# Optimization experiments

Hardware: AMD Instinct MI355X
Metric: run time of the kernel (lower is better)

Reference implementation:

```python
import math
import jax, jax.numpy as jnp
import numpy as np

D_MODEL = 1024
N_HEADS = 16
D_K = D_MODEL // N_HEADS
B = 8
L = 1024
LATTICE = (4, 4)
TWO_PI = 2.0 * math.pi


def _build_neighbors():
    """Replicates LatticeMultiHeadAttention._build_neighbors (Moore 8-neighborhood)."""
    positions = [divmod(i, LATTICE[1]) for i in range(N_HEADS)]
    idx = np.full((N_HEADS, 8), -1, dtype=np.int64)
    w = np.zeros((N_HEADS, 8), dtype=np.float32)
    for i, (r1, c1) in enumerate(positions):
        k = 0
        for dr in (-1, 0, 1):
            for dc in (-1, 0, 1):
                if dr == 0 and dc == 0:
                    continue
                if k >= 8:
                    break
                r2, c2 = r1 + dr, c1 + dc
                for j, (r, c) in enumerate(positions):
                    if (r, c) == (r2, c2):
                        idx[i, k] = j
                        w[i, k] = math.exp(-math.hypot(dr, dc))
                        k += 1
                        break
    return idx, w


def setup_inputs() -> dict:
    key = jax.random.key(0)
    ks = jax.random.split(key, 8)
    s = 1.0 / math.sqrt(D_MODEL)
    nbr_idx_np, nbr_w_np = _build_neighbors()
    return {
        "query": jax.random.normal(ks[0], (B, L, D_MODEL), jnp.float32),
        "key_": jax.random.normal(ks[1], (B, L, D_MODEL), jnp.float32),
        "value": jax.random.normal(ks[2], (B, L, D_MODEL), jnp.float32),
        # head-stacked projection weights, stored as [H, d_model, d_k] (x @ W)
        "Wq": jax.random.normal(ks[3], (N_HEADS, D_MODEL, D_K), jnp.float32) * s,
        "Wk": jax.random.normal(ks[4], (N_HEADS, D_MODEL, D_K), jnp.float32) * s,
        "Wv": jax.random.normal(ks[5], (N_HEADS, D_MODEL, D_K), jnp.float32) * s,
        "Wo": jax.random.normal(ks[6], (D_MODEL, D_MODEL), jnp.float32) * s,
        "bo": jax.random.normal(ks[7], (D_MODEL,), jnp.float32) * 0.01,
        # buffers: initial phases (0.0), intrinsic freqs 1 + 0.1*h, lattice tables
        "phases0": jnp.zeros((N_HEADS,), jnp.float32),
        "freqs": jnp.asarray(1.0 + 0.1 * np.arange(N_HEADS), jnp.float32),
        "nbr_w": jnp.asarray(nbr_w_np),
        "nbr_idx": jnp.asarray(nbr_idx_np),
    }


def _updated_phases(phases0, freqs, nbr_w, nbr_idx):
    # multi-head batched Kuramoto step (note: coupling_strength is NOT used here,
    # matching the original forward), then the per-head internal step (empty
    # neighbor_phases branch adds another 0.01 * intrinsic_freq).
    valid = (nbr_idx >= 0).astype(phases0.dtype)        # [H,8]
    nbr_ph = phases0[jnp.clip(nbr_idx, 0, None)] * valid  # [H,8]
    phase_diff = nbr_ph - phases0[:, None]
    force = (nbr_w * jnp.sin(phase_diff)).sum(axis=1)     # [H]
    p1 = jnp.mod(phases0 + 0.01 * (freqs + force), TWO_PI)
    p2 = jnp.mod(p1 + 0.01 * freqs, TWO_PI)
    return p2


def reference(query, key_, value, Wq, Wk, Wv, Wo, bo, phases0, freqs, nbr_w, nbr_idx):
    # phases are torch buffers updated under no_grad -> constants w.r.t. autodiff
    p2 = jax.lax.stop_gradient(
        _updated_phases(phases0, freqs, nbr_w, nbr_idx))
    bias = 0.1 * jnp.cos(p2)                               # [H]

    Q = jnp.einsum('bld,hdk->bhlk', query, Wq)
    K = jnp.einsum('bld,hdk->bhlk', key_, Wk)
    V = jnp.einsum('bld,hdk->bhlk', value, Wv)

    scores = jnp.einsum('bhlk,bhmk->bhlm', Q, K) / jnp.sqrt(
        jnp.asarray(D_K, Q.dtype))
    scores = scores + bias[None, :, None, None]
    attn = jax.nn.softmax(scores, axis=-1)                 # [B,H,L,L]
    ctx = jnp.einsum('bhlm,bhmk->bhlk', attn, V)           # [B,H,L,d_k]
    ctx = ctx.transpose(0, 2, 1, 3).reshape(query.shape[0], query.shape[1], D_MODEL)
    return ctx @ Wo + bo                                   # out_proj
```

## Files before the change

kernel.cpp:

```cpp
#include <hip/hip_runtime.h>
#include <hip/hip_bf16.h>
#include <stdint.h>


typedef unsigned short u16;
typedef __bf16 bf16_t;
typedef bf16_t bf16x8 __attribute__((ext_vector_type(8)));
typedef u16 u16x8 __attribute__((ext_vector_type(8)));
typedef float f32x4 __attribute__((ext_vector_type(4)));

#define DEVI static __device__ __forceinline__
#define MFMA16(a, b, c) __builtin_amdgcn_mfma_f32_16x16x32_bf16((a), (b), (c), 0, 0, 0)

DEVI void gload_lds16(const void* g, void* l) {
  __builtin_amdgcn_global_load_lds((__attribute__((address_space(1))) void*)g,
                                   (__attribute__((address_space(3))) void*)l, 16, 0, 0);
}

DEVI u16 f2bf(float x) {
  bf16_t b = (bf16_t)x;
  u16 u;
  __builtin_memcpy(&u, &b, 2);
  return u;
}

__global__ __launch_bounds__(256) void prep(const float* __restrict__ Wq,
                                            const float* __restrict__ Wk,
                                            const float* __restrict__ Wv,
                                            const float* __restrict__ Wo,
                                            const float* __restrict__ q,
                                            const float* __restrict__ k,
                                            const float* __restrict__ v,
                                            u16* __restrict__ ws) {
  int bx = blockIdx.x;
  if (bx < 1024) {
    __shared__ float T[64][65];
    int mat = bx >> 8, ti = bx & 255;
    int rb = ti >> 4, cb = ti & 15;
    const float* src = (mat == 0) ? Wq : (mat == 1) ? Wk : (mat == 2) ? Wv : Wo;
    u16* dst = ws + (size_t)mat * 1048576;
    int stride = (mat < 3) ? 64 : 1024;
    size_t srcBase = (mat < 3) ? ((size_t)rb * 65536 + cb * 4096)
                               : ((size_t)rb * 65536 + cb * 64);
    size_t dstBase = (mat < 3) ? ((size_t)rb * 65536 + cb * 64)
                               : ((size_t)cb * 65536 + rb * 64);
#pragma unroll
    for (int p = 0; p < 4; ++p) {
      int e = p * 256 + threadIdx.x;
      int rr = e >> 4, c4 = (e & 15) * 4;
      float4 vv = *(const float4*)(src + srcBase + (size_t)rr * stride + c4);
      T[rr][c4] = vv.x; T[rr][c4 + 1] = vv.y; T[rr][c4 + 2] = vv.z; T[rr][c4 + 3] = vv.w;
    }
    __syncthreads();
#pragma unroll
    for (int p = 0; p < 2; ++p) {
      int e = p * 256 + threadIdx.x;
      int n = e >> 3, c8 = (e & 7) * 8;
      u16x8 o;
#pragma unroll
      for (int i = 0; i < 8; ++i) o[i] = f2bf(T[c8 + i][n]);
      *(u16x8*)(dst + dstBase + (size_t)n * 1024 + c8) = o;
    }
  } else {
    int id = (bx - 1024) * 256 + threadIdx.x;
    int t = id >> 21;
    size_t rem = (size_t)(id & 2097151) * 4;
    const float* src = (t == 0) ? q : (t == 1) ? k : v;
    float4 a = *(const float4*)(src + rem);
    ushort4 st;
    st.x = f2bf(a.x); st.y = f2bf(a.y); st.z = f2bf(a.z); st.w = f2bf(a.w);
    *(ushort4*)(ws + 4194304 + (size_t)t * 8388608 + rem) = st;
  }
}

__global__ __launch_bounds__(256, 2) void gemm_qkv(const u16* __restrict__ WT,
                                                   const u16* __restrict__ X,
                                                   u16* __restrict__ Qw,
                                                   u16* __restrict__ Kw,
                                                   u16* __restrict__ Vw) {
  __shared__ __align__(1024) u16 lds[2][2][8192];
  char* ldsc = (char*)lds;
  int tid = threadIdx.x;
  int wid = tid >> 6, lane = tid & 63, quad = lane >> 4, l16 = lane & 15;
  int wm = wid >> 1, wn = wid & 1;

  int id = blockIdx.x;
  int wgid = (id & 7) * 192 + (id >> 3);
  int mt = wgid & 7;
  int rest = wgid >> 3;
  int nt = rest & 63;
  int z = rest >> 6;
  const u16* Ag = WT + (size_t)z * 1048576 + (size_t)mt * 131072;
  const u16* Bg = X + (size_t)z * 8388608 + (size_t)nt * 131072;
  u16* out = (z == 0) ? Qw : (z == 1) ? Kw : Vw;
  float oscale = (z == 0) ? 0.125f : 1.0f;

  int r0 = tid >> 3;
  int lc = (tid ^ r0) & 7;
  size_t gbase = (size_t)r0 * 1024 + lc * 8;

  int rx = l16 & 7;
  int rowA = wm * 64 + l16;
  int rowB = wn * 64 + l16;

  auto stage = [&](int buf, int kt) {
#pragma unroll
    for (int p = 0; p < 4; ++p)
      gload_lds16(Ag + gbase + (size_t)p * 32768 + kt * 64,
                  ldsc + buf * 32768 + p * 4096 + tid * 16);
#pragma unroll
    for (int p = 0; p < 4; ++p)
      gload_lds16(Bg + gbase + (size_t)p * 32768 + kt * 64,
                  ldsc + buf * 32768 + 16384 + p * 4096 + tid * 16);
  };
  auto rdA = [&](int buf, int mf, int ks) -> bf16x8 {
    return *(const bf16x8*)(ldsc + buf * 32768 + (rowA + mf * 16) * 128 +
                            ((((ks << 2) | quad) ^ rx) << 4));
  };
  auto rdB = [&](int buf, int nf, int ks) -> bf16x8 {
    return *(const bf16x8*)(ldsc + buf * 32768 + 16384 + (rowB + nf * 16) * 128 +
                            ((((ks << 2) | quad) ^ rx) << 4));
  };

  f32x4 acc[4][4];
#pragma unroll
  for (int i = 0; i < 4; ++i)
#pragma unroll
    for (int j = 0; j < 4; ++j) acc[i][j] = {0.f, 0.f, 0.f, 0.f};
  bf16x8 af[4][2], bfr[4][2];

  stage(0, 0);
  stage(1, 1);
  asm volatile("s_waitcnt vmcnt(8)" ::: "memory");
  __builtin_amdgcn_s_barrier();

  for (int t = 0; t < 16; ++t) {
    int cur = t & 1;
#pragma unroll
    for (int mf = 0; mf < 4; ++mf)
#pragma unroll
      for (int ks = 0; ks < 2; ++ks) af[mf][ks] = rdA(cur, mf, ks);
#pragma unroll
    for (int nf = 0; nf < 4; ++nf)
#pragma unroll
      for (int ks = 0; ks < 2; ++ks) bfr[nf][ks] = rdB(cur, nf, ks);
    asm volatile("s_waitcnt lgkmcnt(0)" ::: "memory");
    __builtin_amdgcn_s_barrier();
    if (t < 14) stage(cur, t + 2);
    __builtin_amdgcn_s_setprio(1);
#pragma unroll
    for (int ks = 0; ks < 2; ++ks)
#pragma unroll
      for (int mf = 0; mf < 4; ++mf)
#pragma unroll
        for (int nf = 0; nf < 4; ++nf)
          acc[mf][nf] = MFMA16(af[mf][ks], bfr[nf][ks], acc[mf][nf]);
    __builtin_amdgcn_s_setprio(0);
    if (t < 14)
      asm volatile("s_waitcnt vmcnt(8)" ::: "memory");
    else
      asm volatile("s_waitcnt vmcnt(0)" ::: "memory");
    __builtin_amdgcn_s_barrier();
  }

#pragma unroll
  for (int mf = 0; mf < 4; ++mf) {
    int m = mt * 128 + wm * 64 + mf * 16 + quad * 4;
    int h = m >> 6, dk = m & 63;
#pragma unroll
    for (int nf = 0; nf < 4; ++nf) {
      int n = nt * 128 + wn * 64 + nf * 16 + l16;
      int bb = n >> 10, l = n & 1023;
      f32x4 vv = acc[mf][nf];
      if (z < 2) {
        ushort4 st;
        st.x = f2bf(vv[0] * oscale); st.y = f2bf(vv[1] * oscale);
        st.z = f2bf(vv[2] * oscale); st.w = f2bf(vv[3] * oscale);
        *(ushort4*)(out + ((size_t)((bb * 16 + h) * 1024 + l) * 64 + dk)) = st;
      } else {
        size_t base = ((size_t)((bb * 16 + h) * 64 + dk)) * 1024 + l;
        out[base] = f2bf(vv[0]);
        out[base + 1024] = f2bf(vv[1]);
        out[base + 2048] = f2bf(vv[2]);
        out[base + 3072] = f2bf(vv[3]);
      }
    }
  }
}

__global__ __launch_bounds__(256, 2) void gemm_out(const u16* __restrict__ A,
                                                   const u16* __restrict__ Bx,
                                                   float* __restrict__ outf,
                                                   const float* __restrict__ bias) {
  __shared__ __align__(1024) u16 lds[2][2][8192];
  char* ldsc = (char*)lds;
  int tid = threadIdx.x;
  int wid = tid >> 6, lane = tid & 63, quad = lane >> 4, l16 = lane & 15;
  int wm = wid >> 1, wn = wid & 1;

  int id = blockIdx.x;
  int wgid = (id & 7) * 64 + (id >> 3);
  int mt = wgid & 7;
  int nt = wgid >> 3;
  const u16* Ag = A + (size_t)mt * 131072;
  const u16* Bg = Bx + (size_t)nt * 131072;

  int r0 = tid >> 3;
  int lc = (tid ^ r0) & 7;
  size_t gbase = (size_t)r0 * 1024 + lc * 8;
  int rx = l16 & 7;
  int rowA = wm * 64 + l16;
  int rowB = wn * 64 + l16;

  auto stage = [&](int buf, int kt) {
#pragma unroll
    for (int p = 0; p < 4; ++p)
      gload_lds16(Ag + gbase + (size_t)p * 32768 + kt * 64,
                  ldsc + buf * 32768 + p * 4096 + tid * 16);
#pragma unroll
    for (int p = 0; p < 4; ++p)
      gload_lds16(Bg + gbase + (size_t)p * 32768 + kt * 64,
                  ldsc + buf * 32768 + 16384 + p * 4096 + tid * 16);
  };
  auto rdA = [&](int buf, int mf, int ks) -> bf16x8 {
    return *(const bf16x8*)(ldsc + buf * 32768 + (rowA + mf * 16) * 128 +
                            ((((ks << 2) | quad) ^ rx) << 4));
  };
  auto rdB = [&](int buf, int nf, int ks) -> bf16x8 {
    return *(const bf16x8*)(ldsc + buf * 32768 + 16384 + (rowB + nf * 16) * 128 +
                            ((((ks << 2) | quad) ^ rx) << 4));
  };

  f32x4 acc[4][4];
#pragma unroll
  for (int i = 0; i < 4; ++i)
#pragma unroll
    for (int j = 0; j < 4; ++j) acc[i][j] = {0.f, 0.f, 0.f, 0.f};
  bf16x8 af[4][2], bfr[4][2];

  stage(0, 0);
  stage(1, 1);
  asm volatile("s_waitcnt vmcnt(8)" ::: "memory");
  __builtin_amdgcn_s_barrier();

  for (int t = 0; t < 16; ++t) {
    int cur = t & 1;
#pragma unroll
    for (int mf = 0; mf < 4; ++mf)
#pragma unroll
      for (int ks = 0; ks < 2; ++ks) af[mf][ks] = rdA(cur, mf, ks);
#pragma unroll
    for (int nf = 0; nf < 4; ++nf)
#pragma unroll
      for (int ks = 0; ks < 2; ++ks) bfr[nf][ks] = rdB(cur, nf, ks);
    asm volatile("s_waitcnt lgkmcnt(0)" ::: "memory");
    __builtin_amdgcn_s_barrier();
    if (t < 14) stage(cur, t + 2);
    __builtin_amdgcn_s_setprio(1);
#pragma unroll
    for (int ks = 0; ks < 2; ++ks)
#pragma unroll
      for (int mf = 0; mf < 4; ++mf)
#pragma unroll
        for (int nf = 0; nf < 4; ++nf)
          acc[mf][nf] = MFMA16(af[mf][ks], bfr[nf][ks], acc[mf][nf]);
    __builtin_amdgcn_s_setprio(0);
    if (t < 14)
      asm volatile("s_waitcnt vmcnt(8)" ::: "memory");
    else
      asm volatile("s_waitcnt vmcnt(0)" ::: "memory");
    __builtin_amdgcn_s_barrier();
  }

#pragma unroll
  for (int mf = 0; mf < 4; ++mf) {
    int m = mt * 128 + wm * 64 + mf * 16 + quad * 4;
    float4 bq = *(const float4*)(bias + m);
#pragma unroll
    for (int nf = 0; nf < 4; ++nf) {
      int n = nt * 128 + wn * 64 + nf * 16 + l16;
      f32x4 vv = acc[mf][nf];
      float4 st;
      st.x = vv[0] + bq.x;
      st.y = vv[1] + bq.y;
      st.z = vv[2] + bq.z;
      st.w = vv[3] + bq.w;
      *(float4*)(outf + ((size_t)n * 1024 + m)) = st;
    }
  }
}

__global__ __launch_bounds__(256, 4) void attn_k(const u16* __restrict__ Q,
                                                 const u16* __restrict__ K,
                                                 const u16* __restrict__ VT,
                                                 u16* __restrict__ CTX) {
  __shared__ __align__(16) u16 sQ[128 * 64];
  __shared__ __align__(16) u16 sK[64 * 64];
  __shared__ __align__(16) u16 sV[64 * 64];
  int tid = threadIdx.x;
  int wid = tid >> 6, lane = tid & 63, quad = lane >> 4, l16 = lane & 15;
  int id = blockIdx.x + 8 * blockIdx.y;
  int xcd = id & 7, j = id >> 3;
  int qt = j & 7;
  int bh = xcd * 16 + (j >> 3);
  const u16* Qb = Q + (size_t)bh * 65536;
  const u16* Kb = K + (size_t)bh * 65536;
  const u16* Vb = VT + (size_t)bh * 65536;
  int q0 = qt * 128;

#pragma unroll
  for (int p = 0; p < 4; p++) {
    int cl = p * 256 + tid;
    int r = cl >> 3, c = cl & 7, g = c ^ (r & 7);
    gload_lds16(Qb + (size_t)(q0 + r) * 64 + g * 8, (char*)sQ + (p * 256 + wid * 64) * 16);
  }
  __syncthreads();

  bf16x8 bq[2][2];
#pragma unroll
  for (int qf = 0; qf < 2; qf++) {
    int row = wid * 32 + qf * 16 + l16;
#pragma unroll
    for (int ks = 0; ks < 2; ks++) {
      int ch = (ks * 4 + quad) ^ (row & 7);
      bq[qf][ks] = *(const bf16x8*)((const char*)sQ + row * 128 + ch * 16);
    }
  }

  u16* sPw = sQ + wid * 2048;

  f32x4 oacc[4][2];
#pragma unroll
  for (int i = 0; i < 4; i++) {
    oacc[i][0] = {0.f, 0.f, 0.f, 0.f};
    oacc[i][1] = {0.f, 0.f, 0.f, 0.f};
  }
  float lsum[2] = {0.f, 0.f};

  for (int lk0 = 0; lk0 < 1024; lk0 += 64) {
#pragma unroll
    for (int p = 0; p < 2; p++) {
      int cl = p * 256 + tid;
      int r = cl >> 3, c = cl & 7, g = c ^ (r & 7);
      gload_lds16(Kb + (size_t)(lk0 + r) * 64 + g * 8, (char*)sK + (p * 256 + wid * 64) * 16);
      gload_lds16(Vb + (size_t)r * 1024 + lk0 + g * 8, (char*)sV + (p * 256 + wid * 64) * 16);
    }
    __syncthreads();

    f32x4 s[4][2];
#pragma unroll
    for (int mt = 0; mt < 4; mt++) {
      s[mt][0] = {0.f, 0.f, 0.f, 0.f};
      s[mt][1] = {0.f, 0.f, 0.f, 0.f};
    }
#pragma unroll
    for (int ks = 0; ks < 2; ks++) {
#pragma unroll
      for (int mt = 0; mt < 4; mt++) {
        int row = mt * 16 + l16;
        int ch = (ks * 4 + quad) ^ (row & 7);
        bf16x8 a = *(const bf16x8*)((const char*)sK + row * 128 + ch * 16);
        s[mt][0] = MFMA16(a, bq[0][ks], s[mt][0]);
        s[mt][1] = MFMA16(a, bq[1][ks], s[mt][1]);
      }
    }

#pragma unroll
    for (int qf = 0; qf < 2; qf++) {
      int row = qf * 16 + l16;
#pragma unroll
      for (int mt = 0; mt < 4; mt++) {
        float p0 = __expf(s[mt][qf][0]);
        float p1 = __expf(s[mt][qf][1]);
        float p2 = __expf(s[mt][qf][2]);
        float p3 = __expf(s[mt][qf][3]);
        lsum[qf] += (p0 + p1) + (p2 + p3);
        ushort4 st;
        st.x = f2bf(p0); st.y = f2bf(p1); st.z = f2bf(p2); st.w = f2bf(p3);
        int ch = (2 * mt + (quad >> 1)) ^ (row & 7);
        *(ushort4*)((char*)sPw + row * 128 + ch * 16 + (quad & 1) * 8) = st;
      }
    }
    asm volatile("s_waitcnt lgkmcnt(0)" ::: "memory");

    bf16x8 bp[2][2];
#pragma unroll
    for (int qf = 0; qf < 2; qf++) {
      int row = qf * 16 + l16;
#pragma unroll
      for (int c = 0; c < 2; c++) {
        int ch = (c * 4 + quad) ^ (row & 7);
        bp[qf][c] = *(const bf16x8*)((const char*)sPw + row * 128 + ch * 16);
      }
    }
#pragma unroll
    for (int c = 0; c < 2; c++) {
#pragma unroll
      for (int mt = 0; mt < 4; mt++) {
        int row = mt * 16 + l16;
        int ch = (c * 4 + quad) ^ (row & 7);
        bf16x8 a = *(const bf16x8*)((const char*)sV + row * 128 + ch * 16);
        oacc[mt][0] = MFMA16(a, bp[0][c], oacc[mt][0]);
        oacc[mt][1] = MFMA16(a, bp[1][c], oacc[mt][1]);
      }
    }
    __syncthreads();
  }

#pragma unroll
  for (int qf = 0; qf < 2; qf++) {
    lsum[qf] += __shfl_xor(lsum[qf], 16, 64);
    lsum[qf] += __shfl_xor(lsum[qf], 32, 64);
  }
  float inv0 = 1.f / lsum[0], inv1 = 1.f / lsum[1];

  int b = bh >> 4, h = bh & 15;
#pragma unroll
  for (int qf = 0; qf < 2; qf++) {
    int qg = q0 + wid * 32 + qf * 16 + l16;
    float inv = qf ? inv1 : inv0;
#pragma unroll
    for (int mt = 0; mt < 4; mt++) {
      int dk = mt * 16 + quad * 4;
      ushort4 st;
      st.x = f2bf(oacc[mt][qf][0] * inv);
      st.y = f2bf(oacc[mt][qf][1] * inv);
      st.z = f2bf(oacc[mt][qf][2] * inv);
      st.w = f2bf(oacc[mt][qf][3] * inv);
      *(ushort4*)(CTX + (((size_t)(b * 1024 + qg) * 16 + h) * 64 + dk)) = st;
    }
  }
}

extern "C" void kernel_launch(void* const* d_in, const int* in_sizes, int n_in,
                              void* d_out, int out_size, void* d_ws, size_t ws_size,
                              hipStream_t stream) {
  (void)in_sizes; (void)n_in; (void)out_size;
  const float* query = (const float*)d_in[0];
  const float* key_ = (const float*)d_in[1];
  const float* value = (const float*)d_in[2];
  const float* Wq = (const float*)d_in[3];
  const float* Wk = (const float*)d_in[4];
  const float* Wv = (const float*)d_in[5];
  const float* Wo = (const float*)d_in[6];
  const float* bo = (const float*)d_in[7];

  u16* ws = (u16*)d_ws;
  u16* WT = ws;
  u16* X = ws + 4194304;
  u16* Qw = ws + 29360128;
  u16* Kw = ws + 37748736;
  u16* Vw = ws + 46137344;
  u16* Cw = X;
  float* outp = (float*)d_out;

  prep<<<25600, 256, 0, stream>>>(Wq, Wk, Wv, Wo, query, key_, value, ws);
  gemm_qkv<<<dim3(1536), 256, 0, stream>>>(WT, X, Qw, Kw, Vw);
  attn_k<<<dim3(8, 128), 256, 0, stream>>>(Qw, Kw, Vw, Cw);
  gemm_out<<<dim3(512), 256, 0, stream>>>(WT + 3145728, Cw, outp, bo);
}
```

Measured before the change: 277.6 us.

## Fuse fp32-to-bf16 activation conversion into QKV GEMM B-tile loading

Drops the separate prep pass that converted query/key/value to bf16 in workspace. The QKV GEMM now loads fp32 activations straight into registers, converts them, and writes swizzled bf16 tiles to LDS, with prefetch three k-tiles ahead. The main loop is split into two MFMA halves so the LDS writes overlap compute. This removes a full write and re-read of about 50 MB of bf16 activations. In exchange it doubles the B-operand global read bytes per GEMM tile and raises register pressure.

```diff
diff --git a/kernel.cpp b/kernel.cpp
--- a/kernel.cpp
+++ b/kernel.cpp
@@ -28,53 +28,41 @@
                                             const float* __restrict__ Wk,
                                             const float* __restrict__ Wv,
                                             const float* __restrict__ Wo,
-                                            const float* __restrict__ q,
-                                            const float* __restrict__ k,
-                                            const float* __restrict__ v,
                                             u16* __restrict__ ws) {
+  __shared__ float T[64][65];
   int bx = blockIdx.x;
-  if (bx < 1024) {
-    __shared__ float T[64][65];
-    int mat = bx >> 8, ti = bx & 255;
-    int rb = ti >> 4, cb = ti & 15;
-    const float* src = (mat == 0) ? Wq : (mat == 1) ? Wk : (mat == 2) ? Wv : Wo;
-    u16* dst = ws + (size_t)mat * 1048576;
-    int stride = (mat < 3) ? 64 : 1024;
-    size_t srcBase = (mat < 3) ? ((size_t)rb * 65536 + cb * 4096)
-                               : ((size_t)rb * 65536 + cb * 64);
-    size_t dstBase = (mat < 3) ? ((size_t)rb * 65536 + cb * 64)
-                               : ((size_t)cb * 65536 + rb * 64);
-#pragma unroll
-    for (int p = 0; p < 4; ++p) {
-      int e = p * 256 + threadIdx.x;
-      int rr = e >> 4, c4 = (e & 15) * 4;
-      float4 vv = *(const float4*)(src + srcBase + (size_t)rr * stride + c4);
-      T[rr][c4] = vv.x; T[rr][c4 + 1] = vv.y; T[rr][c4 + 2] = vv.z; T[rr][c4 + 3] = vv.w;
-    }
-    __syncthreads();
-#pragma unroll
-    for (int p = 0; p < 2; ++p) {
-      int e = p * 256 + threadIdx.x;
-      int n = e >> 3, c8 = (e & 7) * 8;
-      u16x8 o;
-#pragma unroll
-      for (int i = 0; i < 8; ++i) o[i] = f2bf(T[c8 + i][n]);
-      *(u16x8*)(dst + dstBase + (size_t)n * 1024 + c8) = o;
-    }
-  } else {
-    int id = (bx - 1024) * 256 + threadIdx.x;
-    int t = id >> 21;
-    size_t rem = (size_t)(id & 2097151) * 4;
-    const float* src = (t == 0) ? q : (t == 1) ? k : v;
-    float4 a = *(const float4*)(src + rem);
-    ushort4 st;
-    st.x = f2bf(a.x); st.y = f2bf(a.y); st.z = f2bf(a.z); st.w = f2bf(a.w);
-    *(ushort4*)(ws + 4194304 + (size_t)t * 8388608 + rem) = st;
+  int mat = bx >> 8, ti = bx & 255;
+  int rb = ti >> 4, cb = ti & 15;
+  const float* src = (mat == 0) ? Wq : (mat == 1) ? Wk : (mat == 2) ? Wv : Wo;
+  u16* dst = ws + (size_t)mat * 1048576;
+  int stride = (mat < 3) ? 64 : 1024;
+  size_t srcBase = (mat < 3) ? ((size_t)rb * 65536 + cb * 4096)
+                             : ((size_t)rb * 65536 + cb * 64);
+  size_t dstBase = (mat < 3) ? ((size_t)rb * 65536 + cb * 64)
+                             : ((size_t)cb * 65536 + rb * 64);
+#pragma unroll
+  for (int p = 0; p < 4; ++p) {
+    int e = p * 256 + threadIdx.x;
+    int rr = e >> 4, c4 = (e & 15) * 4;
+    float4 vv = *(const float4*)(src + srcBase + (size_t)rr * stride + c4);
+    T[rr][c4] = vv.x; T[rr][c4 + 1] = vv.y; T[rr][c4 + 2] = vv.z; T[rr][c4 + 3] = vv.w;
+  }
+  __syncthreads();
+#pragma unroll
+  for (int p = 0; p < 2; ++p) {
+    int e = p * 256 + threadIdx.x;
+    int n = e >> 3, c8 = (e & 7) * 8;
+    u16x8 o;
+#pragma unroll
+    for (int i = 0; i < 8; ++i) o[i] = f2bf(T[c8 + i][n]);
+    *(u16x8*)(dst + dstBase + (size_t)n * 1024 + c8) = o;
   }
 }
 
 __global__ __launch_bounds__(256, 2) void gemm_qkv(const u16* __restrict__ WT,
-                                                   const u16* __restrict__ X,
+                                                   const float* __restrict__ qf,
+                                                   const float* __restrict__ kf,
+                                                   const float* __restrict__ vf,
                                                    u16* __restrict__ Qw,
                                                    u16* __restrict__ Kw,
                                                    u16* __restrict__ Vw) {
@@ -91,27 +79,25 @@
   int nt = rest & 63;
   int z = rest >> 6;
   const u16* Ag = WT + (size_t)z * 1048576 + (size_t)mt * 131072;
-  const u16* Bg = X + (size_t)z * 8388608 + (size_t)nt * 131072;
+  const float* Bg = ((z == 0) ? qf : (z == 1) ? kf : vf) + (size_t)nt * 131072;
   u16* out = (z == 0) ? Qw : (z == 1) ? Kw : Vw;
   float oscale = (z == 0) ? 0.125f : 1.0f;
 
   int r0 = tid >> 3;
-  int lc = (tid ^ r0) & 7;
-  size_t gbase = (size_t)r0 * 1024 + lc * 8;
+  int lcA = (tid ^ r0) & 7;
+  size_t gbaseA = (size_t)r0 * 1024 + lcA * 8;
+  int c8f = (tid & 7) * 8;
+  int wxor = (((tid & 7) ^ (r0 & 7)) << 4);
 
   int rx = l16 & 7;
   int rowA = wm * 64 + l16;
   int rowB = wn * 64 + l16;
 
-  auto stage = [&](int buf, int kt) {
+  auto stageA = [&](int buf, int kt) {
 #pragma unroll
     for (int p = 0; p < 4; ++p)
-      gload_lds16(Ag + gbase + (size_t)p * 32768 + kt * 64,
+      gload_lds16(Ag + gbaseA + (size_t)p * 32768 + kt * 64,
                   ldsc + buf * 32768 + p * 4096 + tid * 16);
-#pragma unroll
-    for (int p = 0; p < 4; ++p)
-      gload_lds16(Bg + gbase + (size_t)p * 32768 + kt * 64,
-                  ldsc + buf * 32768 + 16384 + p * 4096 + tid * 16);
   };
   auto rdA = [&](int buf, int mf, int ks) -> bf16x8 {
     return *(const bf16x8*)(ldsc + buf * 32768 + (rowA + mf * 16) * 128 +
@@ -128,40 +114,96 @@
 #pragma unroll
     for (int j = 0; j < 4; ++j) acc[i][j] = {0.f, 0.f, 0.f, 0.f};
   bf16x8 af[4][2], bfr[4][2];
-
-  stage(0, 0);
-  stage(1, 1);
-  asm volatile("s_waitcnt vmcnt(8)" ::: "memory");
+  float4 fa[8], fb[8];
+
+#define ISSUE_F(KT, F)                                                        \
+  do {                                                                        \
+    _Pragma("unroll") for (int s = 0; s < 4; ++s) {                           \
+      const float* gp = Bg + (size_t)(s * 32 + r0) * 1024 + (KT) * 64 + c8f;  \
+      F[2 * s] = *(const float4*)gp;                                          \
+      F[2 * s + 1] = *(const float4*)(gp + 4);                                \
+    }                                                                         \
+  } while (0)
+
+#define WRITE_B(BUF, F)                                                       \
+  do {                                                                        \
+    _Pragma("unroll") for (int s = 0; s < 4; ++s) {                           \
+      u16x8 o;                                                                \
+      o[0] = f2bf(F[2 * s].x); o[1] = f2bf(F[2 * s].y);                       \
+      o[2] = f2bf(F[2 * s].z); o[3] = f2bf(F[2 * s].w);                       \
+      o[4] = f2bf(F[2 * s + 1].x); o[5] = f2bf(F[2 * s + 1].y);               \
+      o[6] = f2bf(F[2 * s + 1].z); o[7] = f2bf(F[2 * s + 1].w);               \
+      *(u16x8*)(ldsc + (BUF) * 32768 + 16384 + (s * 32 + r0) * 128 + wxor) = o; \
+    }                                                                         \
+  } while (0)
+
+  ISSUE_F(0, fa);
+  ISSUE_F(1, fb);
+  stageA(0, 0);
+  stageA(1, 1);
+  asm volatile("s_waitcnt vmcnt(16)" ::: "memory");
+  WRITE_B(0, fa);
+  ISSUE_F(2, fa);
+  asm volatile("s_waitcnt vmcnt(16)" ::: "memory");
+  WRITE_B(1, fb);
+  asm volatile("s_waitcnt vmcnt(12)" ::: "memory");
+  asm volatile("s_waitcnt lgkmcnt(0)" ::: "memory");
   __builtin_amdgcn_s_barrier();
 
-  for (int t = 0; t < 16; ++t) {
-    int cur = t & 1;
-#pragma unroll
-    for (int mf = 0; mf < 4; ++mf)
-#pragma unroll
-      for (int ks = 0; ks < 2; ++ks) af[mf][ks] = rdA(cur, mf, ks);
-#pragma unroll
-    for (int nf = 0; nf < 4; ++nf)
-#pragma unroll
-      for (int ks = 0; ks < 2; ++ks) bfr[nf][ks] = rdB(cur, nf, ks);
-    asm volatile("s_waitcnt lgkmcnt(0)" ::: "memory");
-    __builtin_amdgcn_s_barrier();
-    if (t < 14) stage(cur, t + 2);
-    __builtin_amdgcn_s_setprio(1);
-#pragma unroll
-    for (int ks = 0; ks < 2; ++ks)
-#pragma unroll
-      for (int mf = 0; mf < 4; ++mf)
-#pragma unroll
-        for (int nf = 0; nf < 4; ++nf)
-          acc[mf][nf] = MFMA16(af[mf][ks], bfr[nf][ks], acc[mf][nf]);
-    __builtin_amdgcn_s_setprio(0);
-    if (t < 14)
-      asm volatile("s_waitcnt vmcnt(8)" ::: "memory");
-    else
-      asm volatile("s_waitcnt vmcnt(0)" ::: "memory");
-    __builtin_amdgcn_s_barrier();
-  }
+#define QKV_ITER(T, FC, FI)                                                   \
+  do {                                                                        \
+    constexpr int t_ = (T);                                                   \
+    constexpr int cur = t_ & 1;                                               \
+    if (t_ < 13) ISSUE_F(t_ + 3, FI);                                         \
+    _Pragma("unroll") for (int mf = 0; mf < 4; ++mf)                          \
+        af[mf][0] = rdA(cur, mf, 0);                                          \
+    _Pragma("unroll") for (int nf = 0; nf < 4; ++nf)                          \
+        bfr[nf][0] = rdB(cur, nf, 0);                                         \
+    _Pragma("unroll") for (int mf = 0; mf < 4; ++mf)                          \
+        af[mf][1] = rdA(cur, mf, 1);                                          \
+    _Pragma("unroll") for (int nf = 0; nf < 4; ++nf)                          \
+        bfr[nf][1] = rdB(cur, nf, 1);                                         \
+    _Pragma("unroll") for (int mf = 0; mf < 4; ++mf)                          \
+        _Pragma("unroll") for (int nf = 0; nf < 4; ++nf)                      \
+            acc[mf][nf] = MFMA16(af[mf][0], bfr[nf][0], acc[mf][nf]);         \
+    asm volatile("s_waitcnt lgkmcnt(0)" ::: "memory");                        \
+    __builtin_amdgcn_s_barrier();                                             \
+    if (t_ < 14) stageA(cur, t_ + 2);                                         \
+    if (t_ < 13)                                                              \
+      asm volatile("s_waitcnt vmcnt(12)" ::: "memory");                       \
+    else if (t_ == 13)                                                        \
+      asm volatile("s_waitcnt vmcnt(4)" ::: "memory");                        \
+    else                                                                      \
+      asm volatile("s_waitcnt vmcnt(0)" ::: "memory");                        \
+    if (t_ < 14) WRITE_B(cur, FC);                                            \
+    __builtin_amdgcn_s_setprio(1);                                            \
+    _Pragma("unroll") for (int mf = 0; mf < 4; ++mf)                          \
+        _Pragma("unroll") for (int nf = 0; nf < 4; ++nf)                      \
+            acc[mf][nf] = MFMA16(af[mf][1], bfr[nf][1], acc[mf][nf]);         \
+    __builtin_amdgcn_s_setprio(0);                                            \
+    asm volatile("s_waitcnt lgkmcnt(0)" ::: "memory");                        \
+    __builtin_amdgcn_s_barrier();                                             \
+  } while (0)
+
+  QKV_ITER(0, fa, fb);
+  QKV_ITER(1, fb, fa);
+  QKV_ITER(2, fa, fb);
+  QKV_ITER(3, fb, fa);
+  QKV_ITER(4, fa, fb);
+  QKV_ITER(5, fb, fa);
+  QKV_ITER(6, fa, fb);
+  QKV_ITER(7, fb, fa);
+  QKV_ITER(8, fa, fb);
+  QKV_ITER(9, fb, fa);
+  QKV_ITER(10, fa, fb);
+  QKV_ITER(11, fb, fa);
+  QKV_ITER(12, fa, fb);
+  QKV_ITER(13, fb, fa);
+  QKV_ITER(14, fa, fb);
+  QKV_ITER(15, fb, fa);
+#undef QKV_ITER
+#undef ISSUE_F
+#undef WRITE_B
 
 #pragma unroll
   for (int mf = 0; mf < 4; ++mf) {
@@ -447,15 +489,14 @@
 
   u16* ws = (u16*)d_ws;
   u16* WT = ws;
-  u16* X = ws + 4194304;
+  u16* Cw = ws + 4194304;
   u16* Qw = ws + 29360128;
   u16* Kw = ws + 37748736;
   u16* Vw = ws + 46137344;
-  u16* Cw = X;
   float* outp = (float*)d_out;
 
-  prep<<<25600, 256, 0, stream>>>(Wq, Wk, Wv, Wo, query, key_, value, ws);
-  gemm_qkv<<<dim3(1536), 256, 0, stream>>>(WT, X, Qw, Kw, Vw);
+  prep<<<1024, 256, 0, stream>>>(Wq, Wk, Wv, Wo, ws);
+  gemm_qkv<<<dim3(1536), 256, 0, stream>>>(WT, query, key_, value, Qw, Kw, Vw);
   attn_k<<<dim3(8, 128), 256, 0, stream>>>(Qw, Kw, Vw, Cw);
   gemm_out<<<dim3(512), 256, 0, stream>>>(WT + 3145728, Cw, outp, bo);
 }
```

Result: slower. 307.5 us (+10.7%).

## Double-buffer K tiles and overlap V loads with QK compute in attention

Applied to the files above, without the earlier changes.

The attention kernel now keeps two K tiles in LDS and prefetches K two tiles ahead. The V tile load is issued at the start of each iteration so it overlaps the QK^T MFMAs and the softmax exponentials. The full __syncthreads are replaced by explicit vmcnt/lgkmcnt waits plus s_barrier, and s_setprio raises wave priority around the MFMA blocks. This aims to hide global-to-LDS latency behind compute, at the cost of 8 KB more LDS per block, which could lower occupancy.

```diff
diff --git a/kernel.cpp b/kernel.cpp
--- a/kernel.cpp
+++ b/kernel.cpp
@@ -295,7 +295,7 @@
                                                  const u16* __restrict__ VT,
                                                  u16* __restrict__ CTX) {
   __shared__ __align__(16) u16 sQ[128 * 64];
-  __shared__ __align__(16) u16 sK[64 * 64];
+  __shared__ __align__(16) u16 sK[2][64 * 64];
   __shared__ __align__(16) u16 sV[64 * 64];
   int tid = threadIdx.x;
   int wid = tid >> 6, lane = tid & 63, quad = lane >> 4, l16 = lane & 15;
@@ -308,13 +308,35 @@
   const u16* Vb = VT + (size_t)bh * 65536;
   int q0 = qt * 128;
 
+  auto stageK = [&](int buf, int lk0) {
+#pragma unroll
+    for (int p = 0; p < 2; ++p) {
+      int cl = p * 256 + tid;
+      int r = cl >> 3, c = cl & 7, g = c ^ (r & 7);
+      gload_lds16(Kb + (size_t)(lk0 + r) * 64 + g * 8,
+                  (char*)sK + buf * 8192 + (p * 256 + wid * 64) * 16);
+    }
+  };
+  auto stageV = [&](int lk0) {
+#pragma unroll
+    for (int p = 0; p < 2; ++p) {
+      int cl = p * 256 + tid;
+      int r = cl >> 3, c = cl & 7, g = c ^ (r & 7);
+      gload_lds16(Vb + (size_t)r * 1024 + lk0 + g * 8,
+                  (char*)sV + (p * 256 + wid * 64) * 16);
+    }
+  };
+
 #pragma unroll
   for (int p = 0; p < 4; p++) {
     int cl = p * 256 + tid;
     int r = cl >> 3, c = cl & 7, g = c ^ (r & 7);
     gload_lds16(Qb + (size_t)(q0 + r) * 64 + g * 8, (char*)sQ + (p * 256 + wid * 64) * 16);
   }
-  __syncthreads();
+  stageK(0, 0);
+  stageK(1, 64);
+  asm volatile("s_waitcnt vmcnt(2)" ::: "memory");
+  __builtin_amdgcn_s_barrier();
 
   bf16x8 bq[2][2];
 #pragma unroll
@@ -337,15 +359,9 @@
   }
   float lsum[2] = {0.f, 0.f};
 
-  for (int lk0 = 0; lk0 < 1024; lk0 += 64) {
-#pragma unroll
-    for (int p = 0; p < 2; p++) {
-      int cl = p * 256 + tid;
-      int r = cl >> 3, c = cl & 7, g = c ^ (r & 7);
-      gload_lds16(Kb + (size_t)(lk0 + r) * 64 + g * 8, (char*)sK + (p * 256 + wid * 64) * 16);
-      gload_lds16(Vb + (size_t)r * 1024 + lk0 + g * 8, (char*)sV + (p * 256 + wid * 64) * 16);
-    }
-    __syncthreads();
+  for (int t = 0; t < 16; ++t) {
+    int cur = t & 1;
+    stageV(t * 64);
 
     f32x4 s[4][2];
 #pragma unroll
@@ -353,17 +369,19 @@
       s[mt][0] = {0.f, 0.f, 0.f, 0.f};
       s[mt][1] = {0.f, 0.f, 0.f, 0.f};
     }
+    __builtin_amdgcn_s_setprio(1);
 #pragma unroll
     for (int ks = 0; ks < 2; ks++) {
 #pragma unroll
       for (int mt = 0; mt < 4; mt++) {
         int row = mt * 16 + l16;
         int ch = (ks * 4 + quad) ^ (row & 7);
-        bf16x8 a = *(const bf16x8*)((const char*)sK + row * 128 + ch * 16);
+        bf16x8 a = *(const bf16x8*)((const char*)sK + cur * 8192 + row * 128 + ch * 16);
         s[mt][0] = MFMA16(a, bq[0][ks], s[mt][0]);
         s[mt][1] = MFMA16(a, bq[1][ks], s[mt][1]);
       }
     }
+    __builtin_amdgcn_s_setprio(0);
 
 #pragma unroll
     for (int qf = 0; qf < 2; qf++) {
@@ -382,7 +400,6 @@
       }
     }
     asm volatile("s_waitcnt lgkmcnt(0)" ::: "memory");
-
     bf16x8 bp[2][2];
 #pragma unroll
     for (int qf = 0; qf < 2; qf++) {
@@ -393,6 +410,11 @@
         bp[qf][c] = *(const bf16x8*)((const char*)sPw + row * 128 + ch * 16);
       }
     }
+    asm volatile("s_waitcnt vmcnt(0)" ::: "memory");
+    __builtin_amdgcn_s_barrier();
+    if (t < 14) stageK(cur, (t + 2) * 64);
+
+    __builtin_amdgcn_s_setprio(1);
 #pragma unroll
     for (int c = 0; c < 2; c++) {
 #pragma unroll
@@ -404,7 +426,9 @@
         oacc[mt][1] = MFMA16(a, bp[1][c], oacc[mt][1]);
       }
     }
-    __syncthreads();
+    __builtin_amdgcn_s_setprio(0);
+    asm volatile("s_waitcnt lgkmcnt(0)" ::: "memory");
+    __builtin_amdgcn_s_barrier();
   }
 
 #pragma unroll
```

New measurement: 277.1 us, median of 2. About the same (-0.2%).

## Load K/V/Q fragments directly from global memory, dropping shared staging and barriers

Applied to the files above, without the earlier changes.

The attention kernel stops staging Q, K and V tiles through LDS with block-wide barriers. Each wave now reads its MFMA operands straight from global memory (relying on L1/L2 reuse across the four waves) and keeps only a small per-wave LDS buffer for the P tile. V loads are issued early to overlap with the QK^T MFMAs, and s_setprio raises wave priority around the MFMA bursts. This removes the __syncthreads and LDS traffic and shrinks LDS for higher occupancy, at the cost of redundant global/L2 reads by every wave and exposed global-load latency.

```diff
diff --git a/kernel.cpp b/kernel.cpp
--- a/kernel.cpp
+++ b/kernel.cpp
@@ -294,9 +294,7 @@
                                                  const u16* __restrict__ K,
                                                  const u16* __restrict__ VT,
                                                  u16* __restrict__ CTX) {
-  __shared__ __align__(16) u16 sQ[128 * 64];
-  __shared__ __align__(16) u16 sK[64 * 64];
-  __shared__ __align__(16) u16 sV[64 * 64];
+  __shared__ __align__(16) u16 sP[4][2048];
   int tid = threadIdx.x;
   int wid = tid >> 6, lane = tid & 63, quad = lane >> 4, l16 = lane & 15;
   int id = blockIdx.x + 8 * blockIdx.y;
@@ -306,28 +304,19 @@
   const u16* Qb = Q + (size_t)bh * 65536;
   const u16* Kb = K + (size_t)bh * 65536;
   const u16* Vb = VT + (size_t)bh * 65536;
-  int q0 = qt * 128;
-
-#pragma unroll
-  for (int p = 0; p < 4; p++) {
-    int cl = p * 256 + tid;
-    int r = cl >> 3, c = cl & 7, g = c ^ (r & 7);
-    gload_lds16(Qb + (size_t)(q0 + r) * 64 + g * 8, (char*)sQ + (p * 256 + wid * 64) * 16);
-  }
-  __syncthreads();
+  int qw = qt * 128 + wid * 32;
 
   bf16x8 bq[2][2];
 #pragma unroll
-  for (int qf = 0; qf < 2; qf++) {
-    int row = wid * 32 + qf * 16 + l16;
-#pragma unroll
-    for (int ks = 0; ks < 2; ks++) {
-      int ch = (ks * 4 + quad) ^ (row & 7);
-      bq[qf][ks] = *(const bf16x8*)((const char*)sQ + row * 128 + ch * 16);
-    }
-  }
-
-  u16* sPw = sQ + wid * 2048;
+  for (int qf = 0; qf < 2; qf++)
+#pragma unroll
+    for (int ks = 0; ks < 2; ks++)
+      bq[qf][ks] = *(const bf16x8*)(Qb + (size_t)(qw + qf * 16 + l16) * 64 +
+                                    ks * 32 + quad * 8);
+
+  u16* sPw = sP[wid];
+  const u16* Kl = Kb + (size_t)l16 * 64 + quad * 8;
+  const u16* Vl = Vb + (size_t)l16 * 1024 + quad * 8;
 
   f32x4 oacc[4][2];
 #pragma unroll
@@ -337,15 +326,12 @@
   }
   float lsum[2] = {0.f, 0.f};
 
-  for (int lk0 = 0; lk0 < 1024; lk0 += 64) {
-#pragma unroll
-    for (int p = 0; p < 2; p++) {
-      int cl = p * 256 + tid;
-      int r = cl >> 3, c = cl & 7, g = c ^ (r & 7);
-      gload_lds16(Kb + (size_t)(lk0 + r) * 64 + g * 8, (char*)sK + (p * 256 + wid * 64) * 16);
-      gload_lds16(Vb + (size_t)r * 1024 + lk0 + g * 8, (char*)sV + (p * 256 + wid * 64) * 16);
-    }
-    __syncthreads();
+  for (int t = 0; t < 16; ++t) {
+    int lk0 = t * 64;
+    bf16x8 va0[4];
+#pragma unroll
+    for (int mt = 0; mt < 4; mt++)
+      va0[mt] = *(const bf16x8*)(Vl + (size_t)mt * 16384 + lk0);
 
     f32x4 s[4][2];
 #pragma unroll
@@ -353,17 +339,16 @@
       s[mt][0] = {0.f, 0.f, 0.f, 0.f};
       s[mt][1] = {0.f, 0.f, 0.f, 0.f};
     }
-#pragma unroll
-    for (int ks = 0; ks < 2; ks++) {
+    __builtin_amdgcn_s_setprio(1);
+#pragma unroll
+    for (int ks = 0; ks < 2; ks++)
 #pragma unroll
       for (int mt = 0; mt < 4; mt++) {
-        int row = mt * 16 + l16;
-        int ch = (ks * 4 + quad) ^ (row & 7);
-        bf16x8 a = *(const bf16x8*)((const char*)sK + row * 128 + ch * 16);
+        bf16x8 a = *(const bf16x8*)(Kl + (size_t)(lk0 + mt * 16) * 64 + ks * 32);
         s[mt][0] = MFMA16(a, bq[0][ks], s[mt][0]);
         s[mt][1] = MFMA16(a, bq[1][ks], s[mt][1]);
       }
-    }
+    __builtin_amdgcn_s_setprio(0);
 
 #pragma unroll
     for (int qf = 0; qf < 2; qf++) {
@@ -393,18 +378,23 @@
         bp[qf][c] = *(const bf16x8*)((const char*)sPw + row * 128 + ch * 16);
       }
     }
-#pragma unroll
-    for (int c = 0; c < 2; c++) {
-#pragma unroll
-      for (int mt = 0; mt < 4; mt++) {
-        int row = mt * 16 + l16;
-        int ch = (c * 4 + quad) ^ (row & 7);
-        bf16x8 a = *(const bf16x8*)((const char*)sV + row * 128 + ch * 16);
-        oacc[mt][0] = MFMA16(a, bp[0][c], oacc[mt][0]);
-        oacc[mt][1] = MFMA16(a, bp[1][c], oacc[mt][1]);
-      }
-    }
-    __syncthreads();
+    bf16x8 va1[4];
+#pragma unroll
+    for (int mt = 0; mt < 4; mt++)
+      va1[mt] = *(const bf16x8*)(Vl + (size_t)mt * 16384 + lk0 + 32);
+
+    __builtin_amdgcn_s_setprio(1);
+#pragma unroll
+    for (int mt = 0; mt < 4; mt++) {
+      oacc[mt][0] = MFMA16(va0[mt], bp[0][0], oacc[mt][0]);
+      oacc[mt][1] = MFMA16(va0[mt], bp[1][0], oacc[mt][1]);
+    }
+#pragma unroll
+    for (int mt = 0; mt < 4; mt++) {
+      oacc[mt][0] = MFMA16(va1[mt], bp[0][1], oacc[mt][0]);
+      oacc[mt][1] = MFMA16(va1[mt], bp[1][1], oacc[mt][1]);
+    }
+    __builtin_amdgcn_s_setprio(0);
   }
 
 #pragma unroll
@@ -417,7 +407,7 @@
   int b = bh >> 4, h = bh & 15;
 #pragma unroll
   for (int qf = 0; qf < 2; qf++) {
-    int qg = q0 + wid * 32 + qf * 16 + l16;
+    int qg = qw + qf * 16 + l16;
     float inv = qf ? inv1 : inv0;
 #pragma unroll
     for (int mt = 0; mt < 4; mt++) {
```

New measurement: 370.7 us. 33.5% more time.
